# Kernel optimization log

Hardware: AMD Instinct MI355X
Metric: run time of the kernel (lower is better)

Reference implementation:

```python
import jax, jax.numpy as jnp
import numpy as np

V, D, H, L, S, B = 32000, 512, 8, 6, 1024, 4
DH = D // H
T_ITERS = 2  # tree_iterations


def _ln(x, w, b, eps=1e-5):
    mu = jnp.mean(x, axis=-1, keepdims=True)
    var = jnp.mean((x - mu) ** 2, axis=-1, keepdims=True)
    return (x - mu) * jax.lax.rsqrt(var + eps) * w + b


def setup_inputs() -> dict:
    key = jax.random.key(0)
    ks = jax.random.split(key, 16)
    std = 0.02
    inp = {
        'input_ids': jax.random.randint(ks[0], (B, S), 0, V),
        'tok_emb': jax.random.normal(ks[1], (V, D), jnp.float32) * std,
        'pos_emb': jax.random.normal(ks[2], (S, D), jnp.float32) * std,
        # attention params, stacked over layers
        'Wq': jax.random.normal(ks[3], (L, D, D), jnp.float32) * std,
        'bq': jnp.zeros((L, D), jnp.float32),
        'Wk': jax.random.normal(ks[4], (L, D, D), jnp.float32) * std,
        'bk': jnp.zeros((L, D), jnp.float32),
        'Wv': jax.random.normal(ks[5], (L, D, D), jnp.float32) * std,
        'bv': jnp.zeros((L, D), jnp.float32),
        'Wo': jax.random.normal(ks[6], (L, D, D), jnp.float32) * std,
        'bo': jnp.zeros((L, D), jnp.float32),
        'ln1w': jnp.ones((L, D), jnp.float32), 'ln1b': jnp.zeros((L, D), jnp.float32),
        'ln2w': jnp.ones((L, D), jnp.float32), 'ln2b': jnp.zeros((L, D), jnp.float32),
        # TreeFFN params: input proj, edge proj (concat src,dst), gate
        'Win': jax.random.normal(ks[7], (L, D, D), jnp.float32) * std,
        'bin_': jnp.zeros((L, D), jnp.float32),
        'Wedge': jax.random.normal(ks[8], (L, 2 * D, D), jnp.float32) * std,
        'bedge': jnp.zeros((L, D), jnp.float32),
        'Wgate': jax.random.normal(ks[9], (L, D, D), jnp.float32) * std,
        'bgate': jnp.zeros((L, D), jnp.float32),
        'lnfw': jnp.ones((D,), jnp.float32), 'lnfb': jnp.zeros((D,), jnp.float32),
        'Whead': jax.random.normal(ks[10], (D, V), jnp.float32) * std,
    }
    return inp


def reference(input_ids, tok_emb, pos_emb, Wq, bq, Wk, bk, Wv, bv, Wo, bo,
              ln1w, ln1b, ln2w, ln2b, Win, bin_, Wedge, bedge, Wgate, bgate,
              lnfw, lnfb, Whead):
    b, s = input_ids.shape
    h = tok_emb[input_ids] + pos_emb[None, :s]  # [B,S,D]
    causal = jnp.tril(jnp.ones((s, s), bool))
    scale = 1.0 / jnp.sqrt(jnp.asarray(DH, h.dtype))
    for l in range(L):
        # --- multi-head self-attention with causal mask ---
        x = _ln(h, ln1w[l], ln1b[l])
        q = (x @ Wq[l] + bq[l]).reshape(b, s, H, DH)
        k = (x @ Wk[l] + bk[l]).reshape(b, s, H, DH)
        v = (x @ Wv[l] + bv[l]).reshape(b, s, H, DH)
        scores = jnp.einsum('bqhd,bkhd->bhqk', q, k) * scale
        scores = jnp.where(causal[None, None], scores, jnp.finfo(scores.dtype).min)
        attn = jax.nn.softmax(scores, axis=-1)
        av = jnp.einsum('bhqk,bkhd->bqhd', attn, v).reshape(b, s, D)
        h = h + av @ Wo[l] + bo[l]
        # --- TreeFFN: sequential-edge (i->i+1) message passing ---
        t = _ln(h, ln2w[l], ln2b[l]) @ Win[l] + bin_[l]
        for _ in range(T_ITERS):
            # edges: src = nodes 0..S-2, dst = nodes 1..S-1
            msg = jax.nn.relu(
                jnp.concatenate([t[:, :-1], t[:, 1:]], axis=-1) @ Wedge[l] + bedge[l]
            )  # [B,S-1,D]
            agg = jnp.pad(msg, ((0, 0), (1, 0), (0, 0)))  # scatter-add at dst nodes
            gate = jax.nn.sigmoid(agg @ Wgate[l] + bgate[l])
            t = t + gate * agg
        h = h + t
    h = _ln(h, lnfw, lnfb)
    return h @ Whead  # [B,S,V]
```

## Files before the change

### kernel.cpp

```cpp
#include <hip/hip_runtime.h>
#include <hip/hip_bf16.h>
#include <stdint.h>

#define V_ 32000
#define D_ 512
#define H_ 8
#define L_ 6
#define S_ 1024
#define B_ 4
#define DH_ 64
#define M_ (B_*S_)

typedef __attribute__((ext_vector_type(8))) short bf16x8;
typedef __attribute__((ext_vector_type(4))) short short4b;
typedef __attribute__((ext_vector_type(4))) float f32x4;

__device__ __forceinline__ short f2bs(float f) {
  union { float f; uint32_t u; } x; x.f = f;
  uint32_t r = (x.u + 0x7FFFu + ((x.u >> 16) & 1u)) >> 16;
  return (short)r;
}
__device__ __forceinline__ float bs2f(short s) {
  union { uint32_t u; float f; } x; x.u = ((uint32_t)(uint16_t)s) << 16;
  return x.f;
}

__device__ __forceinline__ f32x4 mfma16(bf16x8 a, bf16x8 b, f32x4 c) {
  return __builtin_amdgcn_mfma_f32_16x16x32_bf16(a, b, c, 0, 0, 0);
}

__device__ __forceinline__ void gload16(const short* g, char* lds) {
  __builtin_amdgcn_global_load_lds(
      (const __attribute__((address_space(1))) uint32_t*)g,
      (__attribute__((address_space(3))) uint32_t*)lds, 16, 0, 0);
}

template<int N> __device__ __forceinline__ void waitvm() {
  if constexpr (N == 0) asm volatile("s_waitcnt vmcnt(0)" ::: "memory");
  else if constexpr (N == 4) asm volatile("s_waitcnt vmcnt(4)" ::: "memory");
  else if constexpr (N == 6) asm volatile("s_waitcnt vmcnt(6)" ::: "memory");
  else if constexpr (N == 8) asm volatile("s_waitcnt vmcnt(8)" ::: "memory");
}

__global__ __launch_bounds__(256) void transpose_cvt(const float* __restrict__ in,
    short* __restrict__ out, int K, int N, size_t in_slab, size_t out_slab, int orow0) {
  __shared__ float tile[32][33];
  const float* inp = in + (size_t)blockIdx.z * in_slab;
  short* outp = out + (size_t)blockIdx.z * out_slab;
  int kb = blockIdx.y * 32, nb = blockIdx.x * 32;
  int tx = threadIdx.x, ty = threadIdx.y;
  for (int r = ty; r < 32; r += 8) {
    int k = kb + r, n = nb + tx;
    tile[r][tx] = (k < K && n < N) ? inp[(size_t)k * N + n] : 0.f;
  }
  __syncthreads();
  for (int r = ty; r < 32; r += 8) {
    int n = nb + r, k = kb + tx;
    if (n < N && k < K) outp[(size_t)(orow0 + n) * K + k] = f2bs(tile[tx][r]);
  }
}

__global__ __launch_bounds__(256) void pack_qkv_bias(const float* __restrict__ bq,
    const float* __restrict__ bk, const float* __restrict__ bv, float* __restrict__ o) {
  int i = blockIdx.x * 256 + threadIdx.x;
  int l = i / 1536, c = i - l * 1536;
  float v = (c < 512) ? bq[l * 512 + c] : (c < 1024) ? bk[l * 512 + c - 512]
                                                     : bv[l * 512 + c - 1024];
  o[i] = v;
}

__global__ __launch_bounds__(256) void embed_k(const int* __restrict__ ids,
    const float* __restrict__ tok, const float* __restrict__ pos, float* __restrict__ h) {
  int bs = blockIdx.x;
  int tid = threadIdx.x;
  int s = bs & (S_ - 1);
  int id = ids[bs];
  float2 te = *(const float2*)(tok + (size_t)id * D_ + tid * 2);
  float2 pe = *(const float2*)(pos + (size_t)s * D_ + tid * 2);
  float2 r; r.x = te.x + pe.x; r.y = te.y + pe.y;
  *(float2*)(h + (size_t)bs * D_ + tid * 2) = r;
}

__global__ __launch_bounds__(256) void ln4_k(const float* __restrict__ in,
    const float* __restrict__ w, const float* __restrict__ bb, short* __restrict__ outb) {
  int wv = threadIdx.x >> 6, lane = threadIdx.x & 63;
  int row = blockIdx.x * 4 + wv;
  const float* x = in + (size_t)row * D_ + lane * 8;
  float4 v0 = *(const float4*)x;
  float4 v1 = *(const float4*)(x + 4);
  float s = v0.x + v0.y + v0.z + v0.w + v1.x + v1.y + v1.z + v1.w;
  #pragma unroll
  for (int o = 32; o; o >>= 1) s += __shfl_xor(s, o);
  float mu = s * (1.f / D_);
  float d[8] = {v0.x-mu, v0.y-mu, v0.z-mu, v0.w-mu, v1.x-mu, v1.y-mu, v1.z-mu, v1.w-mu};
  float s2 = 0.f;
  #pragma unroll
  for (int j = 0; j < 8; ++j) s2 += d[j] * d[j];
  #pragma unroll
  for (int o = 32; o; o >>= 1) s2 += __shfl_xor(s2, o);
  float rs = rsqrtf(s2 * (1.f / D_) + 1e-5f);
  float4 w0 = *(const float4*)(w + lane * 8);
  float4 w1 = *(const float4*)(w + lane * 8 + 4);
  float4 b0 = *(const float4*)(bb + lane * 8);
  float4 b1 = *(const float4*)(bb + lane * 8 + 4);
  float wj[8] = {w0.x,w0.y,w0.z,w0.w,w1.x,w1.y,w1.z,w1.w};
  float bj[8] = {b0.x,b0.y,b0.z,b0.w,b1.x,b1.y,b1.z,b1.w};
  short o8[8];
  #pragma unroll
  for (int j = 0; j < 8; ++j) o8[j] = f2bs(d[j] * rs * wj[j] + bj[j]);
  *(uint4*)(outb + (size_t)row * D_ + lane * 8) = *(uint4*)o8;
}

template<int AMODE, int EMODE, int BN>
__global__ __launch_bounds__(256) void gemm3_k(
    const short* __restrict__ A, const short* __restrict__ Wt,
    const float* __restrict__ bias, float* __restrict__ Cf,
    short* __restrict__ Cb, const short* __restrict__ Agg,
    float* __restrict__ Hf, const short* __restrict__ zpad,
    int M, int N, int K)
{
  constexpr int NF = BN / 32;
  constexpr int BR = BN / 32;
  constexpr int LOADS = 2 + BR;
  __shared__ __align__(16) char As[2][64 * 128];
  __shared__ __align__(16) char Bs[2][BN * 128];
  const int tid = threadIdx.x;
  const int lane = tid & 63, w = tid >> 6;
  const int m0 = blockIdx.x * 64, n0 = blockIdx.y * BN;
  const int l15 = lane & 15, l4 = lane >> 4;
  const int wm = (w >> 1) * 32, wn = (w & 1) * (BN / 2);

  const int lrow_b = tid >> 3;
  const int kel0 = (tid & 7) * 8;
  const short* agp[2];
  const short* agpHi[2];
  #pragma unroll
  for (int r = 0; r < 2; ++r) {
    int lrow = r * 32 + lrow_b;
    int row = m0 + lrow;
    int kel = kel0 ^ ((lrow & 7) << 3);
    if (AMODE == 0) {
      agp[r] = A + (size_t)row * K + kel;
    } else if (AMODE == 1) {
      agp[r]   = A + (size_t)row * D_ + kel;
      agpHi[r] = ((row & (S_ - 1)) == (S_ - 1)) ? zpad + kel
                                                : A + (size_t)(row + 1) * D_ + kel;
    } else {
      agp[r] = ((row & (S_ - 1)) == 0) ? zpad + kel : A + (size_t)(row - 1) * D_ + kel;
    }
  }
  const short* bgp[BR];
  #pragma unroll
  for (int r = 0; r < BR; ++r) {
    int lrow = r * 32 + lrow_b;
    int kel = kel0 ^ ((lrow & 7) << 3);
    bgp[r] = Wt + (size_t)(n0 + lrow) * K + kel;
  }

  auto stage = [&](int buf, int k0) {
    #pragma unroll
    for (int r = 0; r < 2; ++r) {
      const short* gp;
      if (AMODE == 1) gp = (k0 < D_) ? agp[r] + k0 : agpHi[r] + (k0 - D_);
      else gp = agp[r] + k0;
      gload16(gp, As[buf] + r * 4096 + w * 1024);
    }
    #pragma unroll
    for (int r = 0; r < BR; ++r)
      gload16(bgp[r] + k0, Bs[buf] + r * 4096 + w * 1024);
  };

  const int rswz = (l15 & 7) << 4;
  int aoff[2], boff[NF];
  #pragma unroll
  for (int i = 0; i < 2; ++i) aoff[i] = (wm + i * 16 + l15) * 128;
  #pragma unroll
  for (int j = 0; j < NF; ++j) boff[j] = (wn + j * 16 + l15) * 128;

  f32x4 acc[2][NF] = {};

  const int nk = K >> 6;
  stage(0, 0);
  for (int t = 0; t < nk; ++t) {
    const int cur = t & 1;
    if (t + 1 < nk) { stage(cur ^ 1, (t + 1) * 64); waitvm<LOADS>(); }
    else waitvm<0>();
    __syncthreads();
    #pragma unroll
    for (int kk = 0; kk < 2; ++kk) {
      const int cb = (kk * 64 + l4 * 16) ^ rswz;
      bf16x8 af[2], bfr[NF];
      #pragma unroll
      for (int i = 0; i < 2; ++i) af[i] = *(const bf16x8*)(As[cur] + aoff[i] + cb);
      #pragma unroll
      for (int j = 0; j < NF; ++j) bfr[j] = *(const bf16x8*)(Bs[cur] + boff[j] + cb);
      __builtin_amdgcn_s_setprio(1);
      #pragma unroll
      for (int i = 0; i < 2; ++i)
        #pragma unroll
        for (int j = 0; j < NF; ++j)
          acc[i][j] = mfma16(af[i], bfr[j], acc[i][j]);
      __builtin_amdgcn_s_setprio(0);
    }
    __syncthreads();
  }

  const int rowb = m0 + wm + l4 * 4;
  const int colb = n0 + wn + l15;
  #pragma unroll
  for (int i = 0; i < 2; ++i) {
    #pragma unroll
    for (int j = 0; j < NF; ++j) {
      int col = colb + j * 16;
      float bias_v = bias ? bias[col] : 0.f;
      #pragma unroll
      for (int r = 0; r < 4; ++r) {
        int row = rowb + i * 16 + r;
        size_t idx = (size_t)row * N + col;
        float v = acc[i][j][r] + bias_v;
        if (EMODE == 0) {
          if (Cb) { Cf[idx] = v; Cb[idx] = f2bs(v); }
          else __builtin_nontemporal_store(v, &Cf[idx]);
        } else if (EMODE == 1) {
          Cf[idx] += v;
        } else if (EMODE == 2) {
          Cb[idx] = f2bs(fmaxf(v, 0.f));
        } else if (EMODE == 3) {
          float g = 1.f / (1.f + __expf(-v));
          float aggv = ((row & (S_ - 1)) == 0) ? 0.f : bs2f(Agg[idx - N]);
          float tn = Cf[idx] + g * aggv;
          Cf[idx] = tn; Cb[idx] = f2bs(tn);
        } else if (EMODE == 5) {
          float g = 1.f / (1.f + __expf(-v));
          float aggv = ((row & (S_ - 1)) == 0) ? 0.f : bs2f(Agg[idx - N]);
          Hf[idx] += Cf[idx] + g * aggv;
        } else {
          float sc = (col < D_) ? 0.180336880f : 1.f;
          Cb[idx] = f2bs(v * sc);
        }
      }
    }
  }
}

__global__ __launch_bounds__(256) void gemm2_k(
    const short* __restrict__ A, const short* __restrict__ Wt,
    float* __restrict__ Cf, int M, int N, int K)
{
  __shared__ __align__(16) char As[2][128 * 128];
  __shared__ __align__(16) char Bs[2][128 * 128];
  const int tid = threadIdx.x;
  const int lane = tid & 63, w = tid >> 6;
  const int nwg = gridDim.x * gridDim.y;
  const int bid = blockIdx.x + blockIdx.y * gridDim.x;
  const int swz = (bid & 7) * (nwg >> 3) + (bid >> 3);
  const int m0 = (swz % gridDim.x) * 128, n0 = (swz / gridDim.x) * 128;
  const int l15 = lane & 15, l4 = lane >> 4;
  const int wm = (w >> 1) * 64, wn = (w & 1) * 64;

  const int lrow_b = tid >> 3;
  const int kel0 = (tid & 7) * 8;
  const short* agp[4];
  const short* bgp[4];
  #pragma unroll
  for (int r = 0; r < 4; ++r) {
    int lrow = r * 32 + lrow_b;
    int kel = kel0 ^ ((lrow & 7) << 3);
    agp[r] = A + (size_t)(m0 + lrow) * K + kel;
    bgp[r] = Wt + (size_t)(n0 + lrow) * K + kel;
  }
  auto stage = [&](int buf, int k0) {
    #pragma unroll
    for (int r = 0; r < 4; ++r) gload16(agp[r] + k0, As[buf] + r * 4096 + w * 1024);
    #pragma unroll
    for (int r = 0; r < 4; ++r) gload16(bgp[r] + k0, Bs[buf] + r * 4096 + w * 1024);
  };

  const int rswz = (l15 & 7) << 4;
  int aoff[4], boff[4];
  #pragma unroll
  for (int i = 0; i < 4; ++i) aoff[i] = (wm + i * 16 + l15) * 128;
  #pragma unroll
  for (int j = 0; j < 4; ++j) boff[j] = (wn + j * 16 + l15) * 128;

  f32x4 acc[4][4] = {};
  const int nk = K >> 6;
  stage(0, 0);
  for (int t = 0; t < nk; ++t) {
    const int cur = t & 1;
    if (t + 1 < nk) { stage(cur ^ 1, (t + 1) * 64); waitvm<8>(); }
    else waitvm<0>();
    __syncthreads();
    #pragma unroll
    for (int kk = 0; kk < 2; ++kk) {
      const int cb = (kk * 64 + l4 * 16) ^ rswz;
      bf16x8 af[4], bfr[4];
      #pragma unroll
      for (int i = 0; i < 4; ++i) af[i] = *(const bf16x8*)(As[cur] + aoff[i] + cb);
      #pragma unroll
      for (int j = 0; j < 4; ++j) bfr[j] = *(const bf16x8*)(Bs[cur] + boff[j] + cb);
      __builtin_amdgcn_s_setprio(1);
      #pragma unroll
      for (int i = 0; i < 4; ++i)
        #pragma unroll
        for (int j = 0; j < 4; ++j)
          acc[i][j] = mfma16(af[i], bfr[j], acc[i][j]);
      __builtin_amdgcn_s_setprio(0);
    }
    __syncthreads();
  }

  const int rowb = m0 + wm + l4 * 4;
  const int colb = n0 + wn + l15;
  #pragma unroll
  for (int i = 0; i < 4; ++i)
    #pragma unroll
    for (int j = 0; j < 4; ++j)
      #pragma unroll
      for (int r = 0; r < 4; ++r) {
        size_t idx = (size_t)(rowb + i * 16 + r) * N + colb + j * 16;
        __builtin_nontemporal_store(acc[i][j][r], &Cf[idx]);
      }
}

__global__ __launch_bounds__(256) void fattn_k(const short* __restrict__ Qkv,
    short* __restrict__ avb)
{
  __shared__ short Ks[64][72];
  __shared__ short Vt[64][72];
  __shared__ short Pt[4][16][72];
  const int QS = 3 * D_;
  const int tid = threadIdx.x, lane = tid & 63, w = tid >> 6;
  const int bx = blockIdx.x;
  const int qt = 15 - (bx >> 5);
  const int bh = bx & 31, b = bh >> 3, hh = bh & 7;
  const int l15 = lane & 15, g = lane >> 4;

  const int qrow = qt * 64 + w * 16 + l15;
  const short* qptr = Qkv + (size_t)(b * S_ + qrow) * QS + hh * DH_;
  bf16x8 qa0 = *(const bf16x8*)(qptr + g * 8);
  bf16x8 qa1 = *(const bf16x8*)(qptr + 32 + g * 8);

  f32x4 o[4] = {};
  float mx = -1e30f, lsum = 0.f;

  auto gptr = [&](int kt, int i) {
    int c = tid + i * 256;
    int key = c >> 3, d0 = (c & 7) * 8;
    return Qkv + (size_t)(b * S_ + kt * 64 + key) * QS + hh * DH_ + d0;
  };
  uint4 kvA[2], vvA[2], kvB[2], vvB[2];
  auto load_t = [&](int kt, uint4 kv[2], uint4 vv[2]) {
    #pragma unroll
    for (int i = 0; i < 2; ++i) {
      const short* base = gptr(kt, i);
      kv[i] = *(const uint4*)(base + D_);
      vv[i] = *(const uint4*)(base + 2 * D_);
    }
  };
  auto store_t = [&](uint4 kv[2], uint4 vv[2]) {
    #pragma unroll
    for (int i = 0; i < 2; ++i) {
      int c = tid + i * 256;
      int key = c >> 3, d0 = (c & 7) * 8;
      *(uint4*)&Ks[key][d0] = kv[i];
      short vs[8]; *(uint4*)vs = vv[i];
      int a = (c & 7);
      #pragma unroll
      for (int j = 0; j < 8; ++j)
        Vt[d0 + j][key ^ (a << 3)] = vs[j];
    }
  };

  auto compute = [&](int kt) {
    const int key0 = kt * 64;
    f32x4 sc[4] = {};
    __builtin_amdgcn_s_setprio(1);
    #pragma unroll
    for (int f = 0; f < 4; ++f) {
      bf16x8 ka0 = *(const bf16x8*)&Ks[f * 16 + l15][g * 8];
      bf16x8 ka1 = *(const bf16x8*)&Ks[f * 16 + l15][32 + g * 8];
      sc[f] = mfma16(ka0, qa0, sc[f]);
      sc[f] = mfma16(ka1, qa1, sc[f]);
    }
    __builtin_amdgcn_s_setprio(0);

    float s[16];
    #pragma unroll
    for (int f = 0; f < 4; ++f)
      #pragma unroll
      for (int r = 0; r < 4; ++r)
        s[f * 4 + r] = sc[f][r];
    if (kt == qt) {
      #pragma unroll
      for (int f = 0; f < 4; ++f)
        #pragma unroll
        for (int r = 0; r < 4; ++r)
          if (key0 + f * 16 + g * 4 + r > qrow) s[f * 4 + r] = -1e30f;
    }
    float cm = s[0];
    #pragma unroll
    for (int i = 1; i < 16; ++i) cm = fmaxf(cm, s[i]);
    cm = fmaxf(cm, __shfl_xor(cm, 16));
    cm = fmaxf(cm, __shfl_xor(cm, 32));
    float mn = fmaxf(mx, cm);
    float fr = exp2f(mx - mn);
    mx = mn;
    float p[16], ss = 0.f;
    #pragma unroll
    for (int i = 0; i < 16; ++i) { p[i] = exp2f(s[i] - mn); ss += p[i]; }
    ss += __shfl_xor(ss, 16);
    ss += __shfl_xor(ss, 32);
    lsum = lsum * fr + ss;
    #pragma unroll
    for (int nt = 0; nt < 4; ++nt)
      #pragma unroll
      for (int r = 0; r < 4; ++r) o[nt][r] *= fr;

    #pragma unroll
    for (int f = 0; f < 4; ++f) {
      short tmp[4];
      #pragma unroll
      for (int r = 0; r < 4; ++r) tmp[r] = f2bs(p[f * 4 + r]);
      *(uint2*)&Pt[w][l15][f * 16 + g * 4] = *(uint2*)tmp;
    }
    __builtin_amdgcn_sched_barrier(0);
    bf16x8 pb0 = *(const bf16x8*)&Pt[w][l15][g * 8];
    bf16x8 pb1 = *(const bf16x8*)&Pt[w][l15][32 + g * 8];

    __builtin_amdgcn_s_setprio(1);
    #pragma unroll
    for (int nt = 0; nt < 4; ++nt) {
      int dim = nt * 16 + l15;
      int vswz = ((dim >> 3) & 7) << 3;
      bf16x8 va0 = *(const bf16x8*)&Vt[dim][(g * 8) ^ vswz];
      bf16x8 va1 = *(const bf16x8*)&Vt[dim][(32 + g * 8) ^ vswz];
      o[nt] = mfma16(va0, pb0, o[nt]);
      o[nt] = mfma16(va1, pb1, o[nt]);
    }
    __builtin_amdgcn_s_setprio(0);
  };

  const int ntiles = qt + 1;
  load_t(0, kvA, vvA);
  int kt = 0;
  while (true) {
    __syncthreads();
    store_t(kvA, vvA);
    if (kt + 1 < ntiles) load_t(kt + 1, kvB, vvB);
    __syncthreads();
    compute(kt);
    ++kt; if (kt >= ntiles) break;
    __syncthreads();
    store_t(kvB, vvB);
    if (kt + 1 < ntiles) load_t(kt + 1, kvA, vvA);
    __syncthreads();
    compute(kt);
    ++kt; if (kt >= ntiles) break;
  }

  const float inv = 1.f / lsum;
  #pragma unroll
  for (int nt = 0; nt < 4; ++nt) {
    short ov[4];
    #pragma unroll
    for (int r = 0; r < 4; ++r) ov[r] = f2bs(o[nt][r] * inv);
    *(short4b*)(avb + (size_t)(b * S_ + qrow) * D_ + hh * DH_ + nt * 16 + g * 4) =
        *(short4b*)ov;
  }
}

extern "C" void kernel_launch(void* const* d_in, const int* in_sizes, int n_in,
                              void* d_out, int out_size, void* d_ws, size_t ws_size,
                              hipStream_t stream) {
  const int*   ids   = (const int*)d_in[0];
  const float* tok   = (const float*)d_in[1];
  const float* pos   = (const float*)d_in[2];
  const float* Wq    = (const float*)d_in[3];
  const float* bq    = (const float*)d_in[4];
  const float* Wk    = (const float*)d_in[5];
  const float* bk    = (const float*)d_in[6];
  const float* Wv    = (const float*)d_in[7];
  const float* bv    = (const float*)d_in[8];
  const float* Wo    = (const float*)d_in[9];
  const float* bo    = (const float*)d_in[10];
  const float* ln1w  = (const float*)d_in[11];
  const float* ln1b  = (const float*)d_in[12];
  const float* ln2w  = (const float*)d_in[13];
  const float* ln2b  = (const float*)d_in[14];
  const float* Win   = (const float*)d_in[15];
  const float* bin   = (const float*)d_in[16];
  const float* Wedge = (const float*)d_in[17];
  const float* bedge = (const float*)d_in[18];
  const float* Wgate = (const float*)d_in[19];
  const float* bgate = (const float*)d_in[20];
  const float* lnfw  = (const float*)d_in[21];
  const float* lnfb  = (const float*)d_in[22];
  const float* Whead = (const float*)d_in[23];
  float* out = (float*)d_out;

  char* ws = (char*)d_ws;
  size_t off = 0;
  auto alloc = [&](size_t bytes) {
    void* p = ws + off;
    off = (off + bytes + 255) & ~(size_t)255;
    return p;
  };
  short* wqkv   = (short*)alloc((size_t)L_ * 3 * D_ * D_ * 2);
  float* bqkv   = (float*)alloc((size_t)L_ * 3 * D_ * 4);
  short* wto    = (short*)alloc((size_t)L_ * D_ * D_ * 2);
  short* wtin   = (short*)alloc((size_t)L_ * D_ * D_ * 2);
  short* wtgate = (short*)alloc((size_t)L_ * D_ * D_ * 2);
  short* wtedge = (short*)alloc((size_t)L_ * 2 * D_ * D_ * 2);
  short* wthead = (short*)alloc((size_t)V_ * D_ * 2);
  short* zpad   = (short*)alloc(4096);
  float* hbuf   = (float*)alloc((size_t)M_ * D_ * 4);
  short* xb     = (short*)alloc((size_t)M_ * D_ * 2);
  short* qkvb   = (short*)alloc((size_t)M_ * 3 * D_ * 2);
  short* avb    = (short*)alloc((size_t)M_ * D_ * 2);
  float* tbuf   = (float*)alloc((size_t)M_ * D_ * 4);
  short* tbf    = (short*)alloc((size_t)M_ * D_ * 2);
  short* msgb   = (short*)alloc((size_t)M_ * D_ * 2);
  (void)ws_size; (void)in_sizes; (void)n_in; (void)out_size;

  hipMemsetAsync(zpad, 0, 4096, stream);

  dim3 tblk(32, 8);
  transpose_cvt<<<dim3(16, 16, L_), tblk, 0, stream>>>(Wq, wqkv, D_, D_, (size_t)D_*D_, (size_t)3*D_*D_, 0);
  transpose_cvt<<<dim3(16, 16, L_), tblk, 0, stream>>>(Wk, wqkv, D_, D_, (size_t)D_*D_, (size_t)3*D_*D_, D_);
  transpose_cvt<<<dim3(16, 16, L_), tblk, 0, stream>>>(Wv, wqkv, D_, D_, (size_t)D_*D_, (size_t)3*D_*D_, 2*D_);
  transpose_cvt<<<dim3(16, 16, L_), tblk, 0, stream>>>(Wo, wto, D_, D_, (size_t)D_*D_, (size_t)D_*D_, 0);
  transpose_cvt<<<dim3(16, 16, L_), tblk, 0, stream>>>(Win, wtin, D_, D_, (size_t)D_*D_, (size_t)D_*D_, 0);
  transpose_cvt<<<dim3(16, 16, L_), tblk, 0, stream>>>(Wgate, wtgate, D_, D_, (size_t)D_*D_, (size_t)D_*D_, 0);
  transpose_cvt<<<dim3(16, 32, L_), tblk, 0, stream>>>(Wedge, wtedge, 2*D_, D_, (size_t)2*D_*D_, (size_t)2*D_*D_, 0);
  transpose_cvt<<<dim3(V_/32, 16, 1), tblk, 0, stream>>>(Whead, wthead, D_, V_, (size_t)D_*V_, (size_t)D_*V_, 0);
  pack_qkv_bias<<<(L_ * 3 * D_) / 256, 256, 0, stream>>>(bq, bk, bv, bqkv);

  embed_k<<<M_, 256, 0, stream>>>(ids, tok, pos, hbuf);

  dim3 g64(M_ / 64, D_ / 64);
  dim3 gqkv(M_ / 64, 3 * D_ / 128);
  for (int l = 0; l < L_; ++l) {
    size_t wofs = (size_t)l * D_ * D_;
    ln4_k<<<M_ / 4, 256, 0, stream>>>(hbuf, ln1w + l * D_, ln1b + l * D_, xb);
    gemm3_k<0,4,128><<<gqkv, 256, 0, stream>>>(xb, wqkv + (size_t)l * 3 * D_ * D_,
        bqkv + (size_t)l * 3 * D_, nullptr, qkvb, nullptr, nullptr, zpad, M_, 3 * D_, D_);
    fattn_k<<<B_ * H_ * (S_ / 64), 256, 0, stream>>>(qkvb, avb);
    gemm3_k<0,1,64><<<g64, 256, 0, stream>>>(avb, wto + wofs, bo + l * D_,
        hbuf, nullptr, nullptr, nullptr, zpad, M_, D_, D_);
    ln4_k<<<M_ / 4, 256, 0, stream>>>(hbuf, ln2w + l * D_, ln2b + l * D_, xb);
    gemm3_k<0,0,64><<<g64, 256, 0, stream>>>(xb, wtin + wofs, bin + l * D_,
        tbuf, tbf, nullptr, nullptr, zpad, M_, D_, D_);
    gemm3_k<1,2,64><<<g64, 256, 0, stream>>>(tbf, wtedge + (size_t)l * 2 * D_ * D_,
        bedge + l * D_, nullptr, msgb, nullptr, nullptr, zpad, M_, D_, 2 * D_);
    gemm3_k<2,3,64><<<g64, 256, 0, stream>>>(msgb, wtgate + wofs, bgate + l * D_,
        tbuf, tbf, msgb, nullptr, zpad, M_, D_, D_);
    gemm3_k<1,2,64><<<g64, 256, 0, stream>>>(tbf, wtedge + (size_t)l * 2 * D_ * D_,
        bedge + l * D_, nullptr, msgb, nullptr, nullptr, zpad, M_, D_, 2 * D_);
    gemm3_k<2,5,64><<<g64, 256, 0, stream>>>(msgb, wtgate + wofs, bgate + l * D_,
        tbuf, nullptr, msgb, hbuf, zpad, M_, D_, D_);
  }
  ln4_k<<<M_ / 4, 256, 0, stream>>>(hbuf, lnfw, lnfb, xb);
  gemm2_k<<<dim3(M_ / 128, V_ / 128), 256, 0, stream>>>(xb, wthead, out, M_, V_, D_);
}
```

Measured before the change: 1.005 ms.

## Restructure GEMM and attention pipelines to one barrier per step, stage head-GEMM stores through LDS

The GEMM main loops now issue the next tile's global-to-LDS load, compute on the current buffer, then wait for all loads and sync once per iteration, replacing the earlier partial-vmcnt wait plus two barriers. The head GEMM epilogue writes accumulators into a swizzled LDS tile and then emits coalesced 16-byte nontemporal stores to the large logits output. Flash attention double-buffers K/V in LDS, so the next tile's register-to-LDS store overlaps the current compute and needs only one barrier per step. This uses more LDS in attention and may expose load latency, because the full vmcnt(0) wait now sits after compute.

```diff
diff --git a/kernel.cpp b/kernel.cpp
--- a/kernel.cpp
+++ b/kernel.cpp
@@ -35,11 +35,8 @@
       (__attribute__((address_space(3))) uint32_t*)lds, 16, 0, 0);
 }
 
-template<int N> __device__ __forceinline__ void waitvm() {
-  if constexpr (N == 0) asm volatile("s_waitcnt vmcnt(0)" ::: "memory");
-  else if constexpr (N == 4) asm volatile("s_waitcnt vmcnt(4)" ::: "memory");
-  else if constexpr (N == 6) asm volatile("s_waitcnt vmcnt(6)" ::: "memory");
-  else if constexpr (N == 8) asm volatile("s_waitcnt vmcnt(8)" ::: "memory");
+__device__ __forceinline__ void waitvm0() {
+  asm volatile("s_waitcnt vmcnt(0)" ::: "memory");
 }
 
 __global__ __launch_bounds__(256) void transpose_cvt(const float* __restrict__ in,
@@ -121,7 +118,6 @@
 {
   constexpr int NF = BN / 32;
   constexpr int BR = BN / 32;
-  constexpr int LOADS = 2 + BR;
   __shared__ __align__(16) char As[2][64 * 128];
   __shared__ __align__(16) char Bs[2][BN * 128];
   const int tid = threadIdx.x;
@@ -181,11 +177,12 @@
 
   const int nk = K >> 6;
   stage(0, 0);
+  waitvm0();
+  __syncthreads();
   for (int t = 0; t < nk; ++t) {
     const int cur = t & 1;
-    if (t + 1 < nk) { stage(cur ^ 1, (t + 1) * 64); waitvm<LOADS>(); }
-    else waitvm<0>();
-    __syncthreads();
+    const bool more = (t + 1 < nk);
+    if (more) stage(cur ^ 1, (t + 1) * 64);
     #pragma unroll
     for (int kk = 0; kk < 2; ++kk) {
       const int cb = (kk * 64 + l4 * 16) ^ rswz;
@@ -202,7 +199,10 @@
           acc[i][j] = mfma16(af[i], bfr[j], acc[i][j]);
       __builtin_amdgcn_s_setprio(0);
     }
-    __syncthreads();
+    if (more) {
+      waitvm0();
+      __syncthreads();
+    }
   }
 
   const int rowb = m0 + wm + l4 * 4;
@@ -247,8 +247,9 @@
     const short* __restrict__ A, const short* __restrict__ Wt,
     float* __restrict__ Cf, int M, int N, int K)
 {
-  __shared__ __align__(16) char As[2][128 * 128];
-  __shared__ __align__(16) char Bs[2][128 * 128];
+  __shared__ __align__(16) char smem[65536];
+  char* Asb = smem;
+  char* Bsb = smem + 32768;
   const int tid = threadIdx.x;
   const int lane = tid & 63, w = tid >> 6;
   const int nwg = gridDim.x * gridDim.y;
@@ -271,9 +272,9 @@
   }
   auto stage = [&](int buf, int k0) {
     #pragma unroll
-    for (int r = 0; r < 4; ++r) gload16(agp[r] + k0, As[buf] + r * 4096 + w * 1024);
-    #pragma unroll
-    for (int r = 0; r < 4; ++r) gload16(bgp[r] + k0, Bs[buf] + r * 4096 + w * 1024);
+    for (int r = 0; r < 4; ++r) gload16(agp[r] + k0, Asb + buf * 16384 + r * 4096 + w * 1024);
+    #pragma unroll
+    for (int r = 0; r < 4; ++r) gload16(bgp[r] + k0, Bsb + buf * 16384 + r * 4096 + w * 1024);
   };
 
   const int rswz = (l15 & 7) << 4;
@@ -286,19 +287,22 @@
   f32x4 acc[4][4] = {};
   const int nk = K >> 6;
   stage(0, 0);
+  waitvm0();
+  __syncthreads();
   for (int t = 0; t < nk; ++t) {
     const int cur = t & 1;
-    if (t + 1 < nk) { stage(cur ^ 1, (t + 1) * 64); waitvm<8>(); }
-    else waitvm<0>();
-    __syncthreads();
+    const bool more = (t + 1 < nk);
+    if (more) stage(cur ^ 1, (t + 1) * 64);
     #pragma unroll
     for (int kk = 0; kk < 2; ++kk) {
       const int cb = (kk * 64 + l4 * 16) ^ rswz;
       bf16x8 af[4], bfr[4];
       #pragma unroll
-      for (int i = 0; i < 4; ++i) af[i] = *(const bf16x8*)(As[cur] + aoff[i] + cb);
-      #pragma unroll
-      for (int j = 0; j < 4; ++j) bfr[j] = *(const bf16x8*)(Bs[cur] + boff[j] + cb);
+      for (int i = 0; i < 4; ++i)
+        af[i] = *(const bf16x8*)(Asb + cur * 16384 + aoff[i] + cb);
+      #pragma unroll
+      for (int j = 0; j < 4; ++j)
+        bfr[j] = *(const bf16x8*)(Bsb + cur * 16384 + boff[j] + cb);
       __builtin_amdgcn_s_setprio(1);
       #pragma unroll
       for (int i = 0; i < 4; ++i)
@@ -307,27 +311,41 @@
           acc[i][j] = mfma16(af[i], bfr[j], acc[i][j]);
       __builtin_amdgcn_s_setprio(0);
     }
-    __syncthreads();
-  }
-
-  const int rowb = m0 + wm + l4 * 4;
-  const int colb = n0 + wn + l15;
+    if (more) {
+      waitvm0();
+      __syncthreads();
+    }
+  }
+
+  __syncthreads();
+  float* Lf = (float*)smem;
   #pragma unroll
   for (int i = 0; i < 4; ++i)
     #pragma unroll
     for (int j = 0; j < 4; ++j)
       #pragma unroll
       for (int r = 0; r < 4; ++r) {
-        size_t idx = (size_t)(rowb + i * 16 + r) * N + colb + j * 16;
-        __builtin_nontemporal_store(acc[i][j][r], &Cf[idx]);
+        int row = wm + i * 16 + l4 * 4 + r;
+        int c = wn + j * 16 + l15;
+        int cs = c ^ ((((row & 7) ^ ((c >> 5) & 3))) << 2);
+        Lf[row * 128 + cs] = acc[i][j][r];
       }
+  __syncthreads();
+  #pragma unroll
+  for (int s = 0; s < 16; ++s) {
+    int row = (tid >> 5) + s * 8;
+    int cb = (tid & 31) * 4;
+    int cs = cb ^ ((((row & 7) ^ ((cb >> 5) & 3))) << 2);
+    f32x4 v = *(const f32x4*)&Lf[row * 128 + cs];
+    __builtin_nontemporal_store(v, (f32x4*)&Cf[(size_t)(m0 + row) * N + n0 + cb]);
+  }
 }
 
 __global__ __launch_bounds__(256) void fattn_k(const short* __restrict__ Qkv,
     short* __restrict__ avb)
 {
-  __shared__ short Ks[64][72];
-  __shared__ short Vt[64][72];
+  __shared__ short Ks[2][64][72];
+  __shared__ short Vt[2][64][72];
   __shared__ short Pt[4][16][72];
   const int QS = 3 * D_;
   const int tid = threadIdx.x, lane = tid & 63, w = tid >> 6;
@@ -358,28 +376,28 @@
       vv[i] = *(const uint4*)(base + 2 * D_);
     }
   };
-  auto store_t = [&](uint4 kv[2], uint4 vv[2]) {
+  auto store_t = [&](uint4 kv[2], uint4 vv[2], int bi) {
     #pragma unroll
     for (int i = 0; i < 2; ++i) {
       int c = tid + i * 256;
       int key = c >> 3, d0 = (c & 7) * 8;
-      *(uint4*)&Ks[key][d0] = kv[i];
+      *(uint4*)&Ks[bi][key][d0] = kv[i];
       short vs[8]; *(uint4*)vs = vv[i];
       int a = (c & 7);
       #pragma unroll
       for (int j = 0; j < 8; ++j)
-        Vt[d0 + j][key ^ (a << 3)] = vs[j];
-    }
-  };
-
-  auto compute = [&](int kt) {
+        Vt[bi][d0 + j][key ^ (a << 3)] = vs[j];
+    }
+  };
+
+  auto compute = [&](int kt, int bi) {
     const int key0 = kt * 64;
     f32x4 sc[4] = {};
     __builtin_amdgcn_s_setprio(1);
     #pragma unroll
     for (int f = 0; f < 4; ++f) {
-      bf16x8 ka0 = *(const bf16x8*)&Ks[f * 16 + l15][g * 8];
-      bf16x8 ka1 = *(const bf16x8*)&Ks[f * 16 + l15][32 + g * 8];
+      bf16x8 ka0 = *(const bf16x8*)&Ks[bi][f * 16 + l15][g * 8];
+      bf16x8 ka1 = *(const bf16x8*)&Ks[bi][f * 16 + l15][32 + g * 8];
       sc[f] = mfma16(ka0, qa0, sc[f]);
       sc[f] = mfma16(ka1, qa1, sc[f]);
     }
@@ -433,8 +451,8 @@
     for (int nt = 0; nt < 4; ++nt) {
       int dim = nt * 16 + l15;
       int vswz = ((dim >> 3) & 7) << 3;
-      bf16x8 va0 = *(const bf16x8*)&Vt[dim][(g * 8) ^ vswz];
-      bf16x8 va1 = *(const bf16x8*)&Vt[dim][(32 + g * 8) ^ vswz];
+      bf16x8 va0 = *(const bf16x8*)&Vt[bi][dim][(g * 8) ^ vswz];
+      bf16x8 va1 = *(const bf16x8*)&Vt[bi][dim][(32 + g * 8) ^ vswz];
       o[nt] = mfma16(va0, pb0, o[nt]);
       o[nt] = mfma16(va1, pb1, o[nt]);
     }
@@ -443,20 +461,23 @@
 
   const int ntiles = qt + 1;
   load_t(0, kvA, vvA);
-  int kt = 0;
+  store_t(kvA, vvA, 0);
+  __syncthreads();
+  int kt = 0, cur = 0;
   while (true) {
+    bool more = (kt + 1 < ntiles);
+    if (more) load_t(kt + 1, kvB, vvB);
+    compute(kt, cur);
+    if (more) store_t(kvB, vvB, cur ^ 1);
     __syncthreads();
-    store_t(kvA, vvA);
-    if (kt + 1 < ntiles) load_t(kt + 1, kvB, vvB);
+    ++kt; if (!more) break; cur ^= 1;
+
+    more = (kt + 1 < ntiles);
+    if (more) load_t(kt + 1, kvA, vvA);
+    compute(kt, cur);
+    if (more) store_t(kvA, vvA, cur ^ 1);
     __syncthreads();
-    compute(kt);
-    ++kt; if (kt >= ntiles) break;
-    __syncthreads();
-    store_t(kvB, vvB);
-    if (kt + 1 < ntiles) load_t(kt + 1, kvA, vvA);
-    __syncthreads();
-    compute(kt);
-    ++kt; if (kt >= ntiles) break;
+    ++kt; if (!more) break; cur ^= 1;
   }
 
   const float inv = 1.f / lsum;
@@ -523,7 +544,7 @@
   short* msgb   = (short*)alloc((size_t)M_ * D_ * 2);
   (void)ws_size; (void)in_sizes; (void)n_in; (void)out_size;
 
-  hipMemsetAsync(zpad, 0, 4096, stream);
+  (void)hipMemsetAsync(zpad, 0, 4096, stream);
 
   dim3 tblk(32, 8);
   transpose_cvt<<<dim3(16, 16, L_), tblk, 0, stream>>>(Wq, wqkv, D_, D_, (size_t)D_*D_, (size_t)3*D_*D_, 0);
```

After: 1.085 ms. 7.9% more time.
